# Optimization experiments

Measured on AMD Instinct MI355X. Metric: run time of the kernel, lower is better.

The kernel has to match this reference:

```python
import jax, jax.numpy as jnp
import numpy as np
from jax import lax

B, VLEN, H, DIM, C = 32, 2048, 1024, 1024, 32  # batch, value len, hidden_dim, dim, conv_out_channel


def setup_inputs() -> dict:
    key = jax.random.key(0)
    ks = jax.random.split(key, 13)
    s = 0.02
    return {
        "query": jax.random.normal(ks[0], (B, 1, H), dtype=jnp.float32),
        "value": jax.random.normal(ks[1], (B, VLEN, H), dtype=jnp.float32),
        "prev_attn": jax.random.uniform(ks[2], (B, VLEN), dtype=jnp.float32),
        "conv_w": jax.random.normal(ks[3], (C, 1, 3), dtype=jnp.float32) * s,   # Conv1d weight (out,in,k)
        "conv_b": jax.random.normal(ks[4], (C,), dtype=jnp.float32) * s,
        "w_loc": jax.random.normal(ks[5], (DIM, C), dtype=jnp.float32) * s,     # loc_projection (no bias)
        "w_q": jax.random.normal(ks[6], (DIM, H), dtype=jnp.float32) * s,       # query_projection (no bias)
        "w_v": jax.random.normal(ks[7], (DIM, H), dtype=jnp.float32) * s,       # value_projection (no bias)
        "bias": jax.random.uniform(ks[8], (DIM,), dtype=jnp.float32, minval=-0.1, maxval=0.1),
        "w_score": jax.random.normal(ks[9], (1, DIM), dtype=jnp.float32) * s,   # score_projection weight
        "b_score": jax.random.normal(ks[10], (1,), dtype=jnp.float32) * s,
        "w_out": jax.random.normal(ks[11], (H, 2 * H), dtype=jnp.float32) * s,  # out_projection weight
        "b_out": jax.random.normal(ks[12], (H,), dtype=jnp.float32) * s,
    }


def reference(query, value, prev_attn, conv_w, conv_b, w_loc, w_q, w_v, bias,
              w_score, b_score, w_out, b_out):
    # Location features: Conv1d(1 -> C, k=3, pad=1) over prev_attn, then transpose to (B, V, C)
    conv = lax.conv_general_dilated(
        prev_attn[:, None, :], conv_w, window_strides=(1,), padding=[(1, 1)],
        dimension_numbers=("NCH", "OIH", "NCH"),
    ) + conv_b[None, :, None]                       # (B, C, V)
    conv_feat = jnp.transpose(conv, (0, 2, 1))      # (B, V, C)

    qp = jnp.einsum("bqh,dh->bqd", query, w_q)      # (B, 1, DIM)
    vp = jnp.einsum("bvh,dh->bvd", value, w_v)      # (B, V, DIM)
    lp = jnp.einsum("bvc,dc->bvd", conv_feat, w_loc)

    e = jnp.tanh(qp + vp + lp + bias)               # (B, V, DIM), qp broadcasts over V
    score = jnp.einsum("bvd,d->bv", e, w_score[0]) + b_score[0]  # (B, V)

    # smoothing=True: sigmoid then normalize
    s = jax.nn.sigmoid(score)
    attn = s / jnp.sum(s, axis=-1, keepdims=True)   # (B, V)

    context = jnp.einsum("bv,bvh->bh", attn, value)               # (B, H)
    combined = jnp.concatenate([context[:, None, :], query], axis=2)  # (B, 1, 2H)
    output = jnp.einsum("bqk,hk->bqh", combined, w_out) + b_out       # (B, 1, H)
    return output, attn
```

## Files before the change

kernel.cpp:

```cpp
#include <hip/hip_runtime.h>
#include <hip/hip_bf16.h>
#include <math.h>

#define B_SZ 32
#define VLEN_SZ 2048
#define H_SZ 1024
#define DIM_SZ 1024
#define C_SZ 32

typedef float f32x4 __attribute__((ext_vector_type(4)));
typedef short s16x8 __attribute__((ext_vector_type(8)));
typedef short s16x4 __attribute__((ext_vector_type(4)));
typedef unsigned int u32x4 __attribute__((ext_vector_type(4)));

__device__ __forceinline__ short f2bf(float f) {
  unsigned u = __float_as_uint(f);
  u = (u + 0x7fffu + ((u >> 16) & 1u)) >> 16;
  return (short)u;
}

__device__ __forceinline__ float bf2f(short s) {
  return __uint_as_float(((unsigned)(unsigned short)s) << 16);
}

__device__ __forceinline__ unsigned pack2(float a, float b) {
  return __builtin_amdgcn_perm(__float_as_uint(b), __float_as_uint(a), 0x07060302u);
}

__device__ __forceinline__ float fast_tanh(float x) {
  float z = __expf(2.0f * x);
  return 1.0f - 2.0f / (z + 1.0f);
}

__device__ __forceinline__ void ldg_lds16(const void* g, void* l) {
  __builtin_amdgcn_global_load_lds(
      (const __attribute__((address_space(1))) unsigned int*)g,
      (__attribute__((address_space(3))) unsigned int*)l, 16, 0, 0);
}

__global__ __launch_bounds__(256) void k_prep(
    const float* __restrict__ query, const float* __restrict__ w_q,
    const float* __restrict__ bias, const float* __restrict__ prev,
    const float* __restrict__ conv_w, const float* __restrict__ conv_b,
    const float* __restrict__ w_loc, const float* __restrict__ w_v,
    float* __restrict__ qpb, float* __restrict__ cff, short* __restrict__ wlocb,
    short* __restrict__ wvb, float* __restrict__ score, float* __restrict__ context) {
  int bid = blockIdx.x;
  int t = threadIdx.x;
  if (bid < 8192) {
    int wid = bid * 4 + (t >> 6);
    int lane = t & 63;
    int d = wid >> 5;
    int b = wid & 31;
    const f32x4* q4 = (const f32x4*)(query + (size_t)b * H_SZ);
    const f32x4* w4 = (const f32x4*)(w_q + (size_t)d * H_SZ);
    float acc = 0.f;
#pragma unroll
    for (int it = 0; it < 4; ++it) {
      int k = it * 64 + lane;
      f32x4 a = q4[k], w = w4[k];
      acc += a[0] * w[0] + a[1] * w[1] + a[2] * w[2] + a[3] * w[3];
    }
#pragma unroll
    for (int off = 32; off; off >>= 1) acc += __shfl_xor(acc, off, 64);
    if (lane == 0) qpb[(size_t)b * DIM_SZ + d] = acc + bias[d];
  } else if (bid < 8448) {
    int r = (bid - 8192) * 256 + t;
    int v = r & (VLEN_SZ - 1);
    float p0 = prev[r];
    float pm = (v > 0) ? prev[r - 1] : 0.f;
    float pp = (v < VLEN_SZ - 1) ? prev[r + 1] : 0.f;
    float o[C_SZ];
#pragma unroll
    for (int c = 0; c < C_SZ; ++c)
      o[c] = conv_b[c] + pm * conv_w[c * 3 + 0] + p0 * conv_w[c * 3 + 1] + pp * conv_w[c * 3 + 2];
    f32x4* dst = (f32x4*)(cff + (size_t)r * C_SZ);
#pragma unroll
    for (int g = 0; g < 8; ++g)
      dst[g] = (f32x4){o[4 * g], o[4 * g + 1], o[4 * g + 2], o[4 * g + 3]};
  } else if (bid < 8480) {
    int i = (bid - 8448) * 256 + t;
    f32x4 v = ((const f32x4*)w_loc)[i];
    s16x4 o;
    o[0] = f2bf(v[0]); o[1] = f2bf(v[1]); o[2] = f2bf(v[2]); o[3] = f2bf(v[3]);
    ((s16x4*)wlocb)[i] = o;
  } else if (bid < 9504) {
    int i = (bid - 8480) * 256 + t;
    f32x4 v = ((const f32x4*)w_v)[i];
    s16x4 o;
    o[0] = f2bf(v[0]); o[1] = f2bf(v[1]); o[2] = f2bf(v[2]); o[3] = f2bf(v[3]);
    ((s16x4*)wvb)[i] = o;
  } else if (bid < 9568) {
    int i = (bid - 9504) * 256 + t;
    ((f32x4*)score)[i] = (f32x4){0.f, 0.f, 0.f, 0.f};
  } else {
    int i = (bid - 9568) * 256 + t;
    ((f32x4*)context)[i] = (f32x4){0.f, 0.f, 0.f, 0.f};
  }
}

__global__ __launch_bounds__(256, 4) void k_score(
    const float* __restrict__ value, const short* __restrict__ wvb,
    const short* __restrict__ wlocb, const float* __restrict__ cff,
    const float* __restrict__ qpb, const float* __restrict__ w_score,
    float* __restrict__ score) {
  __shared__ float As[128 * 32];
  __shared__ short Bs[128 * 32];
  __shared__ float sred[4][64];

  int t = threadIdx.x;
  int w = t >> 6, l = t & 63;
  int q = l >> 4, l16 = l & 15;
  int bid = blockIdx.x;
  int x = bid & 7;
  int j = bid >> 3;
  int nt = j & 7;
  int mt = x * 64 + (j >> 3);
  int row0 = mt * 128;
  int d0 = nt * 128;
  int b = row0 >> 11;
  int wm = w >> 1, wn = w & 1;

  int ar = l >> 3;
  int ac = (l & 7) ^ ar;
  const float* gA[4];
  float* lA[4];
#pragma unroll
  for (int s = 0; s < 4; ++s) {
    gA[s] = value + (size_t)(row0 + 32 * w + 8 * s + ar) * H_SZ + ac * 4;
    lA[s] = As + (32 * w + 8 * s) * 32;
  }
  int lr = l >> 2;
  int kc = ((l & 3) ^ ((l >> 3) & 3)) * 8;
  const short* gB0 = wvb + (size_t)(d0 + 32 * w + lr) * H_SZ + kc;
  const short* gB1 = wvb + (size_t)(d0 + 32 * w + 16 + lr) * H_SZ + kc;
  short* lB0 = Bs + (32 * w) * 32;
  short* lB1 = Bs + (32 * w + 16) * 32;

  int h7 = l16 & 7;
  int pA0 = ((2 * q) ^ h7) * 4;
  int pA1 = ((2 * q + 1) ^ h7) * 4;
  int posB = (q ^ ((l16 >> 1) & 3)) * 8;

  f32x4 acc[4][4];
#pragma unroll
  for (int i = 0; i < 4; ++i)
#pragma unroll
    for (int jj = 0; jj < 4; ++jj) acc[i][jj] = (f32x4){0.f, 0.f, 0.f, 0.f};

  for (int kt = 0; kt <= 32; ++kt) {
    if (kt < 32) {
      int k0 = kt * 32;
#pragma unroll
      for (int s = 0; s < 4; ++s) ldg_lds16(gA[s] + k0, lA[s]);
      ldg_lds16(gB0 + (size_t)k0, lB0);
      ldg_lds16(gB1 + (size_t)k0, lB1);
    } else {
#pragma unroll
      for (int s = 0; s < 4; ++s)
        ldg_lds16(cff + (size_t)(row0 + 32 * w + 8 * s + ar) * C_SZ + ac * 4, lA[s]);
      ldg_lds16(wlocb + (size_t)(d0 + 32 * w + lr) * C_SZ + kc, lB0);
      ldg_lds16(wlocb + (size_t)(d0 + 32 * w + 16 + lr) * C_SZ + kc, lB1);
    }
    __syncthreads();

    s16x8 a[4], bb[4];
#pragma unroll
    for (int i = 0; i < 4; ++i) {
      const float* rowp = As + (wm * 64 + i * 16 + l16) * 32;
      f32x4 f0 = *(const f32x4*)(rowp + pA0);
      f32x4 f1 = *(const f32x4*)(rowp + pA1);
      u32x4 pk;
      pk[0] = pack2(f0[0], f0[1]);
      pk[1] = pack2(f0[2], f0[3]);
      pk[2] = pack2(f1[0], f1[1]);
      pk[3] = pack2(f1[2], f1[3]);
      a[i] = *(s16x8*)&pk;
    }
#pragma unroll
    for (int jj = 0; jj < 4; ++jj)
      bb[jj] = *(const s16x8*)(Bs + (wn * 64 + jj * 16 + l16) * 32 + posB);
#pragma unroll
    for (int i = 0; i < 4; ++i)
#pragma unroll
      for (int jj = 0; jj < 4; ++jj)
        acc[i][jj] = __builtin_amdgcn_mfma_f32_16x16x32_bf16(a[i], bb[jj], acc[i][jj], 0, 0, 0);
    __syncthreads();
  }

  float qv[4], wv[4];
#pragma unroll
  for (int jj = 0; jj < 4; ++jj) {
    int d = d0 + wn * 64 + jj * 16 + l16;
    qv[jj] = qpb[(size_t)b * DIM_SZ + d];
    wv[jj] = w_score[d];
  }

#pragma unroll
  for (int i = 0; i < 4; ++i) {
#pragma unroll
    for (int r = 0; r < 4; ++r) {
      float part = 0.f;
#pragma unroll
      for (int jj = 0; jj < 4; ++jj)
        part += fast_tanh(acc[i][jj][r] + qv[jj]) * wv[jj];
      part += __shfl_xor(part, 1);
      part += __shfl_xor(part, 2);
      part += __shfl_xor(part, 4);
      part += __shfl_xor(part, 8);
      if (l16 == 0) sred[w][i * 16 + q * 4 + r] = part;
    }
  }
  __syncthreads();
  if (t < 128) {
    int half = t >> 6;
    float v = sred[half * 2][t & 63] + sred[half * 2 + 1][t & 63];
    atomicAdd(&score[row0 + t], v);
  }
}

__global__ __launch_bounds__(256) void k_ctx(
    const float* __restrict__ score, const float* __restrict__ b_score,
    const float* __restrict__ value, float* __restrict__ attn_out,
    float* __restrict__ context) {
  __shared__ float als[VLEN_SZ];
  __shared__ float red[4];
  int b = blockIdx.x, vc = blockIdx.y, t = threadIdx.x;
  float bs = b_score[0];
  float sv[8];
  float lsum = 0.f;
  int v0 = t * 8;
#pragma unroll
  for (int k = 0; k < 8; ++k) {
    float ps = score[(size_t)b * VLEN_SZ + v0 + k] + bs;
    float s = 1.0f / (1.0f + __expf(-ps));
    sv[k] = s;
    lsum += s;
    als[v0 + k] = s;
  }
#pragma unroll
  for (int off = 32; off; off >>= 1) lsum += __shfl_xor(lsum, off, 64);
  if ((t & 63) == 0) red[t >> 6] = lsum;
  __syncthreads();
  float inv = 1.0f / (red[0] + red[1] + red[2] + red[3]);
  if (vc == 0) {
#pragma unroll
    for (int k = 0; k < 8; ++k)
      attn_out[(size_t)b * VLEN_SZ + v0 + k] = sv[k] * inv;
  }

  int h0 = t * 4;
  int vbase = vc * 256;
  const float* vp = value + ((size_t)b * VLEN_SZ + vbase) * H_SZ + h0;
  const float* av = als + vbase;
  f32x4 acc = (f32x4){0.f, 0.f, 0.f, 0.f};
#pragma unroll 8
  for (int v = 0; v < 256; ++v) {
    f32x4 xv = *(const f32x4*)(vp + (size_t)v * H_SZ);
    float a = av[v];
    acc[0] += a * xv[0]; acc[1] += a * xv[1];
    acc[2] += a * xv[2]; acc[3] += a * xv[3];
  }
#pragma unroll
  for (int k = 0; k < 4; ++k)
    atomicAdd(&context[(size_t)b * H_SZ + h0 + k], acc[k] * inv);
}

__global__ void k_out(const float* __restrict__ context, const float* __restrict__ query,
                      const float* __restrict__ w_out, const float* __restrict__ b_out,
                      float* __restrict__ out) {
  int wid = blockIdx.x * 4 + (threadIdx.x >> 6);
  int lane = threadIdx.x & 63;
  int h = wid >> 5;
  int b = wid & 31;
  const f32x4* w4 = (const f32x4*)(w_out + (size_t)h * 2048);
  const f32x4* c4 = (const f32x4*)(context + (size_t)b * H_SZ);
  const f32x4* q4 = (const f32x4*)(query + (size_t)b * H_SZ);
  float acc = 0.f;
#pragma unroll
  for (int it = 0; it < 8; ++it) {
    int k4 = it * 64 + lane;
    f32x4 w = w4[k4];
    f32x4 c = (k4 < 256) ? c4[k4] : q4[k4 - 256];
    acc += w[0] * c[0] + w[1] * c[1] + w[2] * c[2] + w[3] * c[3];
  }
#pragma unroll
  for (int off = 32; off; off >>= 1) acc += __shfl_xor(acc, off, 64);
  if (lane == 0) out[(size_t)b * H_SZ + h] = acc + b_out[h];
}

extern "C" void kernel_launch(void* const* d_in, const int* in_sizes, int n_in,
                              void* d_out, int out_size, void* d_ws, size_t ws_size,
                              hipStream_t stream) {
  const float* query   = (const float*)d_in[0];
  const float* value   = (const float*)d_in[1];
  const float* prev    = (const float*)d_in[2];
  const float* conv_w  = (const float*)d_in[3];
  const float* conv_b  = (const float*)d_in[4];
  const float* w_loc   = (const float*)d_in[5];
  const float* w_q     = (const float*)d_in[6];
  const float* w_v     = (const float*)d_in[7];
  const float* bias    = (const float*)d_in[8];
  const float* w_score = (const float*)d_in[9];
  const float* b_score = (const float*)d_in[10];
  const float* w_out   = (const float*)d_in[11];
  const float* b_out   = (const float*)d_in[12];

  float* out  = (float*)d_out;
  float* attn = out + B_SZ * H_SZ;

  char* ws = (char*)d_ws;
  float* score   = (float*)(ws);
  float* qpb     = (float*)(ws + (256 << 10));
  float* context = (float*)(ws + (384 << 10));
  short* wvb     = (short*)(ws + (512 << 10));
  short* wlocb   = (short*)(ws + (2560 << 10));
  float* cff     = (float*)(ws + (3 << 20));

  k_prep<<<9600, 256, 0, stream>>>(query, w_q, bias, prev, conv_w, conv_b,
                                   w_loc, w_v, qpb, cff, wlocb, wvb, score, context);
  k_score<<<4096, 256, 0, stream>>>(value, wvb, wlocb, cff, qpb, w_score, score);
  k_ctx<<<dim3(B_SZ, 8), 256, 0, stream>>>(score, b_score, value, attn, context);
  k_out<<<(B_SZ * H_SZ) / 4, 256, 0, stream>>>(context, query, w_out, b_out, out);
}
```

Baseline: 636.1 us.

## Pre-convert value to bf16 in prep so GEMM loads bf16 A tiles

```diff
diff --git a/kernel.cpp b/kernel.cpp
--- a/kernel.cpp
+++ b/kernel.cpp
@@ -39,6 +39,183 @@
 }
 
 __global__ __launch_bounds__(256) void k_prep(
+    const float* __restrict__ query, const float* __restrict__ w_q,
+    const float* __restrict__ bias, const float* __restrict__ prev,
+    const float* __restrict__ conv_w, const float* __restrict__ conv_b,
+    const float* __restrict__ w_loc, const float* __restrict__ w_v,
+    const float* __restrict__ value,
+    float* __restrict__ qpb, short* __restrict__ cfb, short* __restrict__ wlocb,
+    short* __restrict__ wvb, short* __restrict__ vb,
+    float* __restrict__ score, float* __restrict__ context) {
+  int bid = blockIdx.x;
+  int t = threadIdx.x;
+  if (bid < 8192) {
+    int wid = bid * 4 + (t >> 6);
+    int lane = t & 63;
+    int d = wid >> 5;
+    int b = wid & 31;
+    const f32x4* q4 = (const f32x4*)(query + (size_t)b * H_SZ);
+    const f32x4* w4 = (const f32x4*)(w_q + (size_t)d * H_SZ);
+    float acc = 0.f;
+#pragma unroll
+    for (int it = 0; it < 4; ++it) {
+      int k = it * 64 + lane;
+      f32x4 a = q4[k], w = w4[k];
+      acc += a[0] * w[0] + a[1] * w[1] + a[2] * w[2] + a[3] * w[3];
+    }
+#pragma unroll
+    for (int off = 32; off; off >>= 1) acc += __shfl_xor(acc, off, 64);
+    if (lane == 0) qpb[(size_t)b * DIM_SZ + d] = acc + bias[d];
+  } else if (bid < 8448) {
+    int r = (bid - 8192) * 256 + t;
+    int v = r & (VLEN_SZ - 1);
+    float p0 = prev[r];
+    float pm = (v > 0) ? prev[r - 1] : 0.f;
+    float pp = (v < VLEN_SZ - 1) ? prev[r + 1] : 0.f;
+    float o[C_SZ];
+#pragma unroll
+    for (int c = 0; c < C_SZ; ++c)
+      o[c] = conv_b[c] + pm * conv_w[c * 3 + 0] + p0 * conv_w[c * 3 + 1] + pp * conv_w[c * 3 + 2];
+    s16x8* dst = (s16x8*)(cfb + (size_t)r * C_SZ);
+#pragma unroll
+    for (int g = 0; g < 4; ++g) {
+      s16x8 pk;
+#pragma unroll
+      for (int e = 0; e < 8; ++e) pk[e] = f2bf(o[8 * g + e]);
+      dst[g] = pk;
+    }
+  } else if (bid < 8480) {
+    int i = (bid - 8448) * 256 + t;
+    f32x4 v = ((const f32x4*)w_loc)[i];
+    s16x4 o;
+    o[0] = f2bf(v[0]); o[1] = f2bf(v[1]); o[2] = f2bf(v[2]); o[3] = f2bf(v[3]);
+    ((s16x4*)wlocb)[i] = o;
+  } else if (bid < 9504) {
+    int i = (bid - 8480) * 256 + t;
+    f32x4 v = ((const f32x4*)w_v)[i];
+    s16x4 o;
+    o[0] = f2bf(v[0]); o[1] = f2bf(v[1]); o[2] = f2bf(v[2]); o[3] = f2bf(v[3]);
+    ((s16x4*)wvb)[i] = o;
+  } else if (bid < 9568) {
+    int i = (bid - 9504) * 256 + t;
+    ((f32x4*)score)[i] = (f32x4){0.f, 0.f, 0.f, 0.f};
+  } else if (bid < 9600) {
+    int i = (bid - 9568) * 256 + t;
+    ((f32x4*)context)[i] = (f32x4){0.f, 0.f, 0.f, 0.f};
+  } else {
+    size_t i = (size_t)(bid - 9600) * 256 + t;
+    const f32x4* src = (const f32x4*)value;
+    f32x4 v0 = src[2 * i], v1 = src[2 * i + 1];
+    s16x8 o;
+    o[0] = f2bf(v0[0]); o[1] = f2bf(v0[1]); o[2] = f2bf(v0[2]); o[3] = f2bf(v0[3]);
+    o[4] = f2bf(v1[0]); o[5] = f2bf(v1[1]); o[6] = f2bf(v1[2]); o[7] = f2bf(v1[3]);
+    ((s16x8*)vb)[i] = o;
+  }
+}
+
+__global__ __launch_bounds__(256, 4) void k_score(
+    const short* __restrict__ vb, const short* __restrict__ wvb,
+    const short* __restrict__ wlocb, const short* __restrict__ cfb,
+    const float* __restrict__ qpb, const float* __restrict__ w_score,
+    float* __restrict__ score) {
+  __shared__ short As[128 * 32];
+  __shared__ short Bs[128 * 32];
+  __shared__ float sred[4][64];
+
+  int t = threadIdx.x;
+  int w = t >> 6, l = t & 63;
+  int q = l >> 4, l16 = l & 15;
+  int bid = blockIdx.x;
+  int x = bid & 7;
+  int j = bid >> 3;
+  int nt = j & 7;
+  int mt = x * 64 + (j >> 3);
+  int row0 = mt * 128;
+  int d0 = nt * 128;
+  int b = row0 >> 11;
+  int wm = w >> 1, wn = w & 1;
+
+  int lr = l >> 2;
+  int kc = ((l & 3) ^ ((l >> 3) & 3)) * 8;
+  const short* gA0 = vb + (size_t)(row0 + 32 * w + lr) * H_SZ + kc;
+  const short* gA1 = vb + (size_t)(row0 + 32 * w + 16 + lr) * H_SZ + kc;
+  const short* gB0 = wvb + (size_t)(d0 + 32 * w + lr) * H_SZ + kc;
+  const short* gB1 = wvb + (size_t)(d0 + 32 * w + 16 + lr) * H_SZ + kc;
+  short* lA0 = As + (32 * w) * 32;
+  short* lA1 = As + (32 * w + 16) * 32;
+  short* lB0 = Bs + (32 * w) * 32;
+  short* lB1 = Bs + (32 * w + 16) * 32;
+
+  int posf = (q ^ ((l16 >> 1) & 3)) * 8;
+
+  f32x4 acc[4][4];
+#pragma unroll
+  for (int i = 0; i < 4; ++i)
+#pragma unroll
+    for (int jj = 0; jj < 4; ++jj) acc[i][jj] = (f32x4){0.f, 0.f, 0.f, 0.f};
+
+  for (int kt = 0; kt <= 32; ++kt) {
+    if (kt < 32) {
+      int k0 = kt * 32;
+      ldg_lds16(gA0 + k0, lA0);
+      ldg_lds16(gA1 + k0, lA1);
+      ldg_lds16(gB0 + k0, lB0);
+      ldg_lds16(gB1 + k0, lB1);
+    } else {
+      ldg_lds16(cfb + (size_t)(row0 + 32 * w + lr) * C_SZ + kc, lA0);
+      ldg_lds16(cfb + (size_t)(row0 + 32 * w + 16 + lr) * C_SZ + kc, lA1);
+      ldg_lds16(wlocb + (size_t)(d0 + 32 * w + lr) * C_SZ + kc, lB0);
+      ldg_lds16(wlocb + (size_t)(d0 + 32 * w + 16 + lr) * C_SZ + kc, lB1);
+    }
+    __syncthreads();
+
+    s16x8 a[4], bb[4];
+#pragma unroll
+    for (int i = 0; i < 4; ++i)
+      a[i] = *(const s16x8*)(As + (wm * 64 + i * 16 + l16) * 32 + posf);
+#pragma unroll
+    for (int jj = 0; jj < 4; ++jj)
+      bb[jj] = *(const s16x8*)(Bs + (wn * 64 + jj * 16 + l16) * 32 + posf);
+#pragma unroll
+    for (int i = 0; i < 4; ++i)
+#pragma unroll
+      for (int jj = 0; jj < 4; ++jj)
+        acc[i][jj] = __builtin_amdgcn_mfma_f32_16x16x32_bf16(a[i], bb[jj], acc[i][jj], 0, 0, 0);
+    __syncthreads();
+  }
+
+  float qv[4], wv[4];
+#pragma unroll
+  for (int jj = 0; jj < 4; ++jj) {
+    int d = d0 + wn * 64 + jj * 16 + l16;
+    qv[jj] = qpb[(size_t)b * DIM_SZ + d];
+    wv[jj] = w_score[d];
+  }
+
+#pragma unroll
+  for (int i = 0; i < 4; ++i) {
+#pragma unroll
+    for (int r = 0; r < 4; ++r) {
+      float part = 0.f;
+#pragma unroll
+      for (int jj = 0; jj < 4; ++jj)
+        part += fast_tanh(acc[i][jj][r] + qv[jj]) * wv[jj];
+      part += __shfl_xor(part, 1);
+      part += __shfl_xor(part, 2);
+      part += __shfl_xor(part, 4);
+      part += __shfl_xor(part, 8);
+      if (l16 == 0) sred[w][i * 16 + q * 4 + r] = part;
+    }
+  }
+  __syncthreads();
+  if (t < 128) {
+    int half = t >> 6;
+    float v = sred[half * 2][t & 63] + sred[half * 2 + 1][t & 63];
+    atomicAdd(&score[row0 + t], v);
+  }
+}
+
+__global__ __launch_bounds__(256) void k_prep_f32(
     const float* __restrict__ query, const float* __restrict__ w_q,
     const float* __restrict__ bias, const float* __restrict__ prev,
     const float* __restrict__ conv_w, const float* __restrict__ conv_b,
@@ -99,7 +276,7 @@
   }
 }
 
-__global__ __launch_bounds__(256, 4) void k_score(
+__global__ __launch_bounds__(256, 4) void k_score_f32(
     const float* __restrict__ value, const short* __restrict__ wvb,
     const short* __restrict__ wlocb, const float* __restrict__ cff,
     const float* __restrict__ qpb, const float* __restrict__ w_score,
@@ -250,12 +427,12 @@
   }
 
   int h0 = t * 4;
-  int vbase = vc * 256;
+  int vbase = vc * 128;
   const float* vp = value + ((size_t)b * VLEN_SZ + vbase) * H_SZ + h0;
   const float* av = als + vbase;
   f32x4 acc = (f32x4){0.f, 0.f, 0.f, 0.f};
 #pragma unroll 8
-  for (int v = 0; v < 256; ++v) {
+  for (int v = 0; v < 128; ++v) {
     f32x4 xv = *(const f32x4*)(vp + (size_t)v * H_SZ);
     float a = av[v];
     acc[0] += a * xv[0]; acc[1] += a * xv[1];
@@ -315,11 +492,21 @@
   float* context = (float*)(ws + (384 << 10));
   short* wvb     = (short*)(ws + (512 << 10));
   short* wlocb   = (short*)(ws + (2560 << 10));
-  float* cff     = (float*)(ws + (3 << 20));
-
-  k_prep<<<9600, 256, 0, stream>>>(query, w_q, bias, prev, conv_w, conv_b,
-                                   w_loc, w_v, qpb, cff, wlocb, wvb, score, context);
-  k_score<<<4096, 256, 0, stream>>>(value, wvb, wlocb, cff, qpb, w_score, score);
-  k_ctx<<<dim3(B_SZ, 8), 256, 0, stream>>>(score, b_score, value, attn, context);
+
+  size_t need = ((size_t)16 << 20) + ((size_t)128 << 20);
+  if (ws_size >= need) {
+    short* cfb = (short*)(ws + (3 << 20));
+    short* vb  = (short*)(ws + ((size_t)16 << 20));
+    k_prep<<<42368, 256, 0, stream>>>(query, w_q, bias, prev, conv_w, conv_b,
+                                      w_loc, w_v, value, qpb, cfb, wlocb, wvb, vb,
+                                      score, context);
+    k_score<<<4096, 256, 0, stream>>>(vb, wvb, wlocb, cfb, qpb, w_score, score);
+  } else {
+    float* cff = (float*)(ws + (3 << 20));
+    k_prep_f32<<<9600, 256, 0, stream>>>(query, w_q, bias, prev, conv_w, conv_b,
+                                         w_loc, w_v, qpb, cff, wlocb, wvb, score, context);
+    k_score_f32<<<4096, 256, 0, stream>>>(value, wvb, wlocb, cff, qpb, w_score, score);
+  }
+  k_ctx<<<dim3(B_SZ, 16), 256, 0, stream>>>(score, b_score, value, attn, context);
   k_out<<<(B_SZ * H_SZ) / 4, 256, 0, stream>>>(context, query, w_out, b_out, out);
 }
```

Result: slower. 657.9 us (+3.4%).
